# Optimization experiments

Measured on AMD Instinct MI355X. Metric: run time of the kernel, lower is better.

## Reference

```python
import jax, jax.numpy as jnp
import numpy as np

N_NODES = 50000
N_EDGES = 800000
F_IN, F_HID, F_OUT = 128, 256, 10


def setup_inputs() -> dict:
    key = jax.random.key(0)
    ks = jax.random.split(key, 8)
    x = jax.random.normal(ks[0], (N_NODES, F_IN), dtype=jnp.float32)
    edge_index = jax.random.randint(ks[1], (2, N_EDGES), 0, N_NODES, dtype=jnp.int64)
    # Glorot-ish init for GCNConv weights (PyG GCNConv: lin weight [in,out] + bias [out])
    def glorot(k, fi, fo):
        s = (6.0 / (fi + fo)) ** 0.5
        return jax.random.uniform(k, (fi, fo), minval=-s, maxval=s, dtype=jnp.float32)
    return {
        "x": x,
        "edge_index": edge_index,
        "W1": glorot(ks[2], F_IN, F_HID), "b1": jnp.zeros((F_HID,), jnp.float32),
        "W2": glorot(ks[3], F_HID, F_HID), "b2": jnp.zeros((F_HID,), jnp.float32),
        "W3": glorot(ks[4], F_HID, F_OUT), "b3": jnp.zeros((F_OUT,), jnp.float32),
    }


def _gcn_conv(x, W, b, src, dst, norm, n_nodes):
    # GCNConv: out[dst] += norm_e * (x @ W)[src]; then + bias
    xw = x @ W                                   # [N, F_out]
    msgs = norm[:, None] * xw[src]               # [E+N, F_out] gather
    agg = jax.ops.segment_sum(msgs, dst, num_segments=n_nodes)
    return agg + b


def reference(x, edge_index, W1, b1, W2, b2, W3, b3):
    n = x.shape[0]
    loops = jnp.arange(n, dtype=edge_index.dtype)
    src = jnp.concatenate([edge_index[0], loops])  # source nodes (messages from)
    dst = jnp.concatenate([edge_index[1], loops])  # target nodes (aggregate into)
    # symmetric normalization D^{-1/2} (A+I) D^{-1/2}, degree from target index
    deg = jax.ops.segment_sum(jnp.ones_like(dst, dtype=x.dtype), dst, num_segments=n)
    dinv = jnp.where(deg > 0, jax.lax.rsqrt(deg), 0.0)
    norm = dinv[src] * dinv[dst]

    h = _gcn_conv(x, W1, b1, src, dst, norm, n)
    h = jax.nn.relu(h)                  # dropout is identity in eval mode
    h = _gcn_conv(h, W2, b2, src, dst, norm, n)
    h = jax.nn.relu(h)
    h = _gcn_conv(h, W3, b3, src, dst, norm, n)
    return jax.nn.log_softmax(h, axis=1)
```

## Files before the change

### kernel.cpp

```cpp
#include <hip/hip_runtime.h>
#include <hip/hip_bf16.h>
#include <math.h>

#define F_IN 128
#define F_HID 256
#define F_OUT 10

typedef __attribute__((ext_vector_type(4))) short s16x4;
typedef __attribute__((ext_vector_type(8))) short s16x8;
typedef __attribute__((ext_vector_type(4))) float f32x4;

static __device__ __forceinline__ float b2f(unsigned short u) {
    union { float f; unsigned int u; } c;
    c.u = ((unsigned int)u) << 16;
    return c.f;
}
static __device__ __forceinline__ unsigned short f2b(float f) {
    return __bfloat16_as_ushort(__float2bfloat16(f));
}


__global__ void count_kernel(const int* __restrict__ dst, int* __restrict__ cnt, int e) {
    int i = blockIdx.x * blockDim.x + threadIdx.x;
    if (i < e) atomicAdd(&cnt[dst[i]], 1);
}

__global__ void dinv_kernel(const int* __restrict__ cnt, float* __restrict__ dinv, int n) {
    int i = blockIdx.x * blockDim.x + threadIdx.x;
    if (i < n) dinv[i] = rsqrtf((float)(cnt[i] + 1));
}

__global__ void scan1_kernel(const int* __restrict__ cnt, int* __restrict__ rowstart,
                             int* __restrict__ partial, int n) {
    __shared__ int s[256];
    int tid = threadIdx.x;
    int i = blockIdx.x * 256 + tid;
    int v = (i < n) ? cnt[i] : 0;
    s[tid] = v;
    __syncthreads();
    for (int off = 1; off < 256; off <<= 1) {
        int t = (tid >= off) ? s[tid - off] : 0;
        __syncthreads();
        s[tid] += t;
        __syncthreads();
    }
    if (i < n) rowstart[i] = s[tid] - v;
    if (tid == 255) partial[blockIdx.x] = s[255];
}

__global__ void scan2_kernel(int* __restrict__ partial, int nb) {
    __shared__ int s[256];
    int tid = threadIdx.x;
    int v = (tid < nb) ? partial[tid] : 0;
    s[tid] = v;
    __syncthreads();
    for (int off = 1; off < 256; off <<= 1) {
        int t = (tid >= off) ? s[tid - off] : 0;
        __syncthreads();
        s[tid] += t;
        __syncthreads();
    }
    if (tid < nb) partial[tid] = s[tid] - v;
}

__global__ void scan3_kernel(int* __restrict__ rowstart, const int* __restrict__ partial,
                             int n, int e) {
    int i = blockIdx.x * blockDim.x + threadIdx.x;
    if (i < n) rowstart[i] += partial[blockIdx.x];
    if (i == 0) rowstart[n] = e;
}

__global__ void fill_kernel(const int* __restrict__ src, const int* __restrict__ dst,
                            const int* __restrict__ rowstart, int* __restrict__ cursor,
                            const float* __restrict__ dinv, int* __restrict__ csr_src,
                            float* __restrict__ csr_norm, int e) {
    int i = blockIdx.x * blockDim.x + threadIdx.x;
    if (i >= e) return;
    int s = src[i], d = dst[i];
    int pos = rowstart[d] + atomicAdd(&cursor[d], 1);
    csr_src[pos] = s;
    csr_norm[pos] = dinv[s] * dinv[d];
}


__global__ void cast_kernel(const float* __restrict__ in, unsigned short* __restrict__ out,
                            size_t total) {
    size_t i = (size_t)(blockIdx.x * blockDim.x + threadIdx.x) * 4;
    if (i >= total) return;
    float4 v = *(const float4*)&in[i];
    ushort4 o;
    o.x = f2b(v.x); o.y = f2b(v.y); o.z = f2b(v.z); o.w = f2b(v.w);
    *(ushort4*)&out[i] = o;
}

__global__ void castT_kernel(const float* __restrict__ in, unsigned short* __restrict__ out,
                             int Kd, int Nd) {
    int i = blockIdx.x * blockDim.x + threadIdx.x;
    if (i >= Kd * Nd) return;
    int k = i / Nd, nn = i - k * Nd;
    out[nn * Kd + k] = f2b(in[i]);
}


template <int F>
__global__ __launch_bounds__(256) void agg_bf16_kernel(const unsigned short* __restrict__ feat,
                                                       const int* __restrict__ rowstart,
                                                       const int* __restrict__ csr_src,
                                                       const float* __restrict__ csr_norm,
                                                       const float* __restrict__ dinv,
                                                       unsigned short* __restrict__ out, int n) {
    constexpr int VEC = F / 64;
    int wid = threadIdx.x >> 6;
    int lane = threadIdx.x & 63;
    int v = blockIdx.x * 4 + wid;
    if (v >= n) return;

    float d = dinv[v];
    float sw = d * d;
    float acc[VEC];

    auto loadrow = [&](int node, float (&dst)[VEC]) {
        const unsigned short* p = feat + (size_t)node * F + lane * VEC;
        if constexpr (VEC == 4) {
            ushort4 t = *(const ushort4*)p;
            dst[0] = b2f(t.x); dst[1] = b2f(t.y); dst[2] = b2f(t.z); dst[3] = b2f(t.w);
        } else {
            ushort2 t = *(const ushort2*)p;
            dst[0] = b2f(t.x); dst[1] = b2f(t.y);
        }
    };

    {
        float t[VEC];
        loadrow(v, t);
#pragma unroll
        for (int j = 0; j < VEC; ++j) acc[j] = sw * t[j];
    }

    int e0 = rowstart[v], e1 = rowstart[v + 1];
    int e = e0;
    for (; e + 8 <= e1; e += 8) {
        int s[8];
        float w[8];
#pragma unroll
        for (int u = 0; u < 8; ++u) {
            s[u] = csr_src[e + u];
            w[u] = csr_norm[e + u];
        }
        float fv[8][VEC];
#pragma unroll
        for (int u = 0; u < 8; ++u) loadrow(s[u], fv[u]);
#pragma unroll
        for (int u = 0; u < 8; ++u)
#pragma unroll
            for (int j = 0; j < VEC; ++j) acc[j] += w[u] * fv[u][j];
    }
    for (; e + 4 <= e1; e += 4) {
        int s[4];
        float w[4];
#pragma unroll
        for (int u = 0; u < 4; ++u) {
            s[u] = csr_src[e + u];
            w[u] = csr_norm[e + u];
        }
        float fv[4][VEC];
#pragma unroll
        for (int u = 0; u < 4; ++u) loadrow(s[u], fv[u]);
#pragma unroll
        for (int u = 0; u < 4; ++u)
#pragma unroll
            for (int j = 0; j < VEC; ++j) acc[j] += w[u] * fv[u][j];
    }
    for (; e < e1; ++e) {
        int s = csr_src[e];
        float w = csr_norm[e];
        float fv[VEC];
        loadrow(s, fv);
#pragma unroll
        for (int j = 0; j < VEC; ++j) acc[j] += w * fv[j];
    }

    unsigned short* po = out + (size_t)v * F + lane * VEC;
    if constexpr (VEC == 4) {
        ushort4 o;
        o.x = f2b(acc[0]); o.y = f2b(acc[1]); o.z = f2b(acc[2]); o.w = f2b(acc[3]);
        *(ushort4*)po = o;
    } else {
        ushort2 o;
        o.x = f2b(acc[0]); o.y = f2b(acc[1]);
        *(ushort2*)po = o;
    }
}


template <int K, bool RELU, bool BF16OUT>
__global__ __launch_bounds__(256) void gemm_mfma_kernel(const unsigned short* __restrict__ A,
                                                        const unsigned short* __restrict__ Bt,
                                                        const float* __restrict__ bias,
                                                        float* __restrict__ C,
                                                        unsigned short* __restrict__ Cb,
                                                        int M, int N) {
    __shared__ unsigned short As[64][40];
    __shared__ unsigned short Bs[64][40];
    int tid = threadIdx.x;
    int w = tid >> 6;
    int lane = tid & 63;
    int g = lane >> 4;
    int r16 = lane & 15;
    int bm = blockIdx.x, bn = blockIdx.y;

    int srow = tid >> 2;
    int scol = (tid & 3) * 8;
    int garow = bm * 64 + srow;
    int gbrow = bn * 64 + srow;

    f32x4 acc[4] = {};

    for (int k0 = 0; k0 < K; k0 += 32) {
        uint4 av = make_uint4(0, 0, 0, 0);
        if (garow < M) av = *(const uint4*)&A[(size_t)garow * K + k0 + scol];
        uint4 bv = *(const uint4*)&Bt[(size_t)gbrow * K + k0 + scol];
        __syncthreads();
        *(uint4*)&As[srow][scol] = av;
        *(uint4*)&Bs[srow][scol] = bv;
        __syncthreads();

        union U { s16x8 v; s16x4 h[2]; };
        U af;
        int arow = w * 16 + r16;
        af.h[0] = *(const s16x4*)&As[arow][g * 4];
        af.h[1] = *(const s16x4*)&As[arow][g * 4 + 16];
#pragma unroll
        for (int cg = 0; cg < 4; ++cg) {
            U bf;
            bf.h[0] = *(const s16x4*)&Bs[cg * 16 + r16][g * 4];
            bf.h[1] = *(const s16x4*)&Bs[cg * 16 + r16][g * 4 + 16];
            acc[cg] = __builtin_amdgcn_mfma_f32_16x16x32_bf16(af.v, bf.v, acc[cg], 0, 0, 0);
        }
    }

#pragma unroll
    for (int cg = 0; cg < 4; ++cg) {
        int col = bn * 64 + cg * 16 + r16;
        float bs = bias[col];
#pragma unroll
        for (int r = 0; r < 4; ++r) {
            int row = bm * 64 + w * 16 + g * 4 + r;
            if (row < M) {
                float v = acc[cg][r] + bs;
                if (RELU) v = fmaxf(v, 0.f);
                if (BF16OUT) {
                    Cb[(size_t)row * N + col] = f2b(v);
                } else {
                    C[(size_t)row * N + col] = v;
                }
            }
        }
    }
}


__global__ void gemm3_kernel(const float* __restrict__ h, const float* __restrict__ W3,
                             float* __restrict__ hw3, int M) {
    __shared__ float w[F_HID * F_OUT];
    for (int i = threadIdx.x; i < F_HID * F_OUT; i += blockDim.x) w[i] = W3[i];
    __syncthreads();
    int r = blockIdx.x * blockDim.x + threadIdx.x;
    if (r >= M) return;
    float acc[F_OUT] = {};
    const float* row = &h[(size_t)r * F_HID];
    for (int k = 0; k < F_HID; k += 4) {
        float4 hv = *(const float4*)&row[k];
#pragma unroll
        for (int j = 0; j < F_OUT; ++j) {
            acc[j] += hv.x * w[(k + 0) * F_OUT + j];
            acc[j] += hv.y * w[(k + 1) * F_OUT + j];
            acc[j] += hv.z * w[(k + 2) * F_OUT + j];
            acc[j] += hv.w * w[(k + 3) * F_OUT + j];
        }
    }
#pragma unroll
    for (int j = 0; j < F_OUT; ++j) hw3[(size_t)r * F_OUT + j] = acc[j];
}


__global__ void final_kernel(const float* __restrict__ hw3, const int* __restrict__ rowstart,
                             const int* __restrict__ csr_src, const float* __restrict__ csr_norm,
                             const float* __restrict__ dinv, const float* __restrict__ b3,
                             float* __restrict__ out, int n) {
    int v = blockIdx.x * blockDim.x + threadIdx.x;
    if (v >= n) return;
    float acc[F_OUT];
    float d = dinv[v];
    float sw = d * d;
#pragma unroll
    for (int j = 0; j < F_OUT; ++j) acc[j] = sw * hw3[(size_t)v * F_OUT + j];
    int e0 = rowstart[v], e1 = rowstart[v + 1];
    for (int e = e0; e < e1; ++e) {
        int s = csr_src[e];
        float w = csr_norm[e];
#pragma unroll
        for (int j = 0; j < F_OUT; ++j) acc[j] += w * hw3[(size_t)s * F_OUT + j];
    }
#pragma unroll
    for (int j = 0; j < F_OUT; ++j) acc[j] += b3[j];
    float m = acc[0];
#pragma unroll
    for (int j = 1; j < F_OUT; ++j) m = fmaxf(m, acc[j]);
    float sum = 0.f;
#pragma unroll
    for (int j = 0; j < F_OUT; ++j) sum += expf(acc[j] - m);
    float lse = m + logf(sum);
#pragma unroll
    for (int j = 0; j < F_OUT; ++j) out[(size_t)v * F_OUT + j] = acc[j] - lse;
}


extern "C" void kernel_launch(void* const* d_in, const int* in_sizes, int n_in,
                              void* d_out, int out_size, void* d_ws, size_t ws_size,
                              hipStream_t stream) {
    const float* x  = (const float*)d_in[0];
    const int*   ei = (const int*)d_in[1];
    const float* W1 = (const float*)d_in[2];
    const float* b1 = (const float*)d_in[3];
    const float* W2 = (const float*)d_in[4];
    const float* b2 = (const float*)d_in[5];
    const float* W3 = (const float*)d_in[6];
    const float* b3 = (const float*)d_in[7];
    float* out = (float*)d_out;

    int n = in_sizes[0] / F_IN;
    int e = in_sizes[1] / 2;
    const int* srcp = ei;
    const int* dstp = ei + e;

    size_t off = 0;
    auto alloc = [&](size_t bytes) -> char* {
        char* p = (char*)d_ws + off;
        off += (bytes + 255) & ~(size_t)255;
        return p;
    };
    int*   cnt      = (int*)alloc((size_t)n * 4);
    int*   cursor   = (int*)alloc((size_t)n * 4);
    int*   rowstart = (int*)alloc((size_t)(n + 1) * 4);
    int*   partial  = (int*)alloc(1024 * 4);
    int*   csr_src  = (int*)alloc((size_t)e * 4);
    float* csr_norm = (float*)alloc((size_t)e * 4);
    float* dinv     = (float*)alloc((size_t)n * 4);
    unsigned short* xb   = (unsigned short*)alloc((size_t)n * F_IN * 2);
    unsigned short* aggb = (unsigned short*)alloc((size_t)n * F_HID * 2);
    unsigned short* h1b  = (unsigned short*)alloc((size_t)n * F_HID * 2);
    unsigned short* W1t  = (unsigned short*)alloc((size_t)F_IN * F_HID * 2);
    unsigned short* W2t  = (unsigned short*)alloc((size_t)F_HID * F_HID * 2);
    float* h2  = (float*)alloc((size_t)n * F_HID * 4);
    float* hw3 = (float*)alloc((size_t)n * F_OUT * 4);

    const int TB = 256;
    hipMemsetAsync(cnt, 0, (size_t)n * 4, stream);
    hipMemsetAsync(cursor, 0, (size_t)n * 4, stream);

    count_kernel<<<(e + TB - 1) / TB, TB, 0, stream>>>(dstp, cnt, e);
    dinv_kernel<<<(n + TB - 1) / TB, TB, 0, stream>>>(cnt, dinv, n);
    int nb = (n + TB - 1) / TB;
    scan1_kernel<<<nb, TB, 0, stream>>>(cnt, rowstart, partial, n);
    scan2_kernel<<<1, TB, 0, stream>>>(partial, nb);
    scan3_kernel<<<nb, TB, 0, stream>>>(rowstart, partial, n, e);
    fill_kernel<<<(e + TB - 1) / TB, TB, 0, stream>>>(srcp, dstp, rowstart, cursor, dinv,
                                                      csr_src, csr_norm, e);

    size_t xtotal = (size_t)n * F_IN;
    cast_kernel<<<(int)((xtotal / 4 + TB - 1) / TB), TB, 0, stream>>>(x, xb, xtotal);
    castT_kernel<<<(F_IN * F_HID + TB - 1) / TB, TB, 0, stream>>>(W1, W1t, F_IN, F_HID);
    castT_kernel<<<(F_HID * F_HID + TB - 1) / TB, TB, 0, stream>>>(W2, W2t, F_HID, F_HID);

    int nwave = (n + 3) / 4;
    dim3 gg((n + 63) / 64, F_HID / 64);

    agg_bf16_kernel<F_IN><<<nwave, 256, 0, stream>>>(xb, rowstart, csr_src, csr_norm, dinv,
                                                     aggb, n);
    gemm_mfma_kernel<F_IN, true, true><<<gg, 256, 0, stream>>>(aggb, W1t, b1, nullptr, h1b,
                                                               n, F_HID);

    agg_bf16_kernel<F_HID><<<nwave, 256, 0, stream>>>(h1b, rowstart, csr_src, csr_norm, dinv,
                                                      aggb, n);
    gemm_mfma_kernel<F_HID, true, false><<<gg, 256, 0, stream>>>(aggb, W2t, b2, h2, nullptr,
                                                                 n, F_HID);

    gemm3_kernel<<<(n + TB - 1) / TB, TB, 0, stream>>>(h2, W3, hw3, n);
    final_kernel<<<(n + TB - 1) / TB, TB, 0, stream>>>(hw3, rowstart, csr_src, csr_norm, dinv,
                                                       b3, out, n);
}
```

Before: 282.6 us.

## Fuse prep kernels, pack CSR src/norm, and split aggregation across feature chunks

Merges the degree count, the x cast and both weight transposes into one multi-job launch, and folds the dinv computation into the first scan pass. The memsets are merged into one, relying on cursor directly following cnt in the workspace. CSR source indices and norms are interleaved into one int2 array. Aggregation now launches a grid over 32-feature column slices, with four edge lanes per feature pair that are reduced by shuffles. This is meant to cut launch count and raise parallelism in the gather, at the cost of re-reading the edge list once per feature slice.

```diff
diff --git a/kernel.cpp b/kernel.cpp
--- a/kernel.cpp
+++ b/kernel.cpp
@@ -20,18 +20,38 @@
 }
 
 
-__global__ void count_kernel(const int* __restrict__ dst, int* __restrict__ cnt, int e) {
+__global__ void prep_kernel(const int* __restrict__ dst, int* __restrict__ cnt, int e,
+                            const float* __restrict__ x, unsigned short* __restrict__ xb,
+                            int xq,
+                            const float* __restrict__ W1, unsigned short* __restrict__ W1t,
+                            const float* __restrict__ W2, unsigned short* __restrict__ W2t) {
     int i = blockIdx.x * blockDim.x + threadIdx.x;
-    if (i < e) atomicAdd(&cnt[dst[i]], 1);
-}
-
-__global__ void dinv_kernel(const int* __restrict__ cnt, float* __restrict__ dinv, int n) {
-    int i = blockIdx.x * blockDim.x + threadIdx.x;
-    if (i < n) dinv[i] = rsqrtf((float)(cnt[i] + 1));
-}
+    int job = blockIdx.y;
+    if (job == 0) {
+        if (i < e) atomicAdd(&cnt[dst[i]], 1);
+    } else if (job == 1) {
+        if (i < xq) {
+            float4 v = *(const float4*)&x[(size_t)i * 4];
+            ushort4 o;
+            o.x = f2b(v.x); o.y = f2b(v.y); o.z = f2b(v.z); o.w = f2b(v.w);
+            *(ushort4*)&xb[(size_t)i * 4] = o;
+        }
+    } else if (job == 2) {
+        if (i < F_IN * F_HID) {
+            int k = i / F_HID, nn = i - k * F_HID;
+            W1t[nn * F_IN + k] = f2b(W1[i]);
+        }
+    } else {
+        if (i < F_HID * F_HID) {
+            int k = i / F_HID, nn = i - k * F_HID;
+            W2t[nn * F_HID + k] = f2b(W2[i]);
+        }
+    }
+}
+
 
 __global__ void scan1_kernel(const int* __restrict__ cnt, int* __restrict__ rowstart,
-                             int* __restrict__ partial, int n) {
+                             int* __restrict__ partial, float* __restrict__ dinv, int n) {
     __shared__ int s[256];
     int tid = threadIdx.x;
     int i = blockIdx.x * 256 + tid;
@@ -44,7 +64,10 @@
         s[tid] += t;
         __syncthreads();
     }
-    if (i < n) rowstart[i] = s[tid] - v;
+    if (i < n) {
+        rowstart[i] = s[tid] - v;
+        dinv[i] = rsqrtf((float)(v + 1));
+    }
     if (tid == 255) partial[blockIdx.x] = s[255];
 }
 
@@ -72,123 +95,69 @@
 
 __global__ void fill_kernel(const int* __restrict__ src, const int* __restrict__ dst,
                             const int* __restrict__ rowstart, int* __restrict__ cursor,
-                            const float* __restrict__ dinv, int* __restrict__ csr_src,
-                            float* __restrict__ csr_norm, int e) {
+                            const float* __restrict__ dinv, int2* __restrict__ pack, int e) {
     int i = blockIdx.x * blockDim.x + threadIdx.x;
     if (i >= e) return;
     int s = src[i], d = dst[i];
     int pos = rowstart[d] + atomicAdd(&cursor[d], 1);
-    csr_src[pos] = s;
-    csr_norm[pos] = dinv[s] * dinv[d];
-}
-
-
-__global__ void cast_kernel(const float* __restrict__ in, unsigned short* __restrict__ out,
-                            size_t total) {
-    size_t i = (size_t)(blockIdx.x * blockDim.x + threadIdx.x) * 4;
-    if (i >= total) return;
-    float4 v = *(const float4*)&in[i];
-    ushort4 o;
-    o.x = f2b(v.x); o.y = f2b(v.y); o.z = f2b(v.z); o.w = f2b(v.w);
-    *(ushort4*)&out[i] = o;
-}
-
-__global__ void castT_kernel(const float* __restrict__ in, unsigned short* __restrict__ out,
-                             int Kd, int Nd) {
-    int i = blockIdx.x * blockDim.x + threadIdx.x;
-    if (i >= Kd * Nd) return;
-    int k = i / Nd, nn = i - k * Nd;
-    out[nn * Kd + k] = f2b(in[i]);
+    float w = dinv[s] * dinv[d];
+    pack[pos] = make_int2(s, __float_as_int(w));
 }
 
 
 template <int F>
-__global__ __launch_bounds__(256) void agg_bf16_kernel(const unsigned short* __restrict__ feat,
-                                                       const int* __restrict__ rowstart,
-                                                       const int* __restrict__ csr_src,
-                                                       const float* __restrict__ csr_norm,
-                                                       const float* __restrict__ dinv,
-                                                       unsigned short* __restrict__ out, int n) {
-    constexpr int VEC = F / 64;
+__global__ __launch_bounds__(256) void agg_split_kernel(const unsigned short* __restrict__ feat,
+                                                        const int* __restrict__ rowstart,
+                                                        const int2* __restrict__ pack,
+                                                        const float* __restrict__ dinv,
+                                                        unsigned short* __restrict__ out,
+                                                        int n) {
     int wid = threadIdx.x >> 6;
     int lane = threadIdx.x & 63;
     int v = blockIdx.x * 4 + wid;
     if (v >= n) return;
+    int esub = lane >> 4;
+    int fidx = lane & 15;
+    int fbase = blockIdx.y * 32;
+    const unsigned short* fcol = feat + fbase + fidx * 2;
 
     float d = dinv[v];
-    float sw = d * d;
-    float acc[VEC];
-
-    auto loadrow = [&](int node, float (&dst)[VEC]) {
-        const unsigned short* p = feat + (size_t)node * F + lane * VEC;
-        if constexpr (VEC == 4) {
-            ushort4 t = *(const ushort4*)p;
-            dst[0] = b2f(t.x); dst[1] = b2f(t.y); dst[2] = b2f(t.z); dst[3] = b2f(t.w);
-        } else {
-            ushort2 t = *(const ushort2*)p;
-            dst[0] = b2f(t.x); dst[1] = b2f(t.y);
-        }
-    };
-
+    float sw = (esub == 0) ? d * d : 0.f;
+    float a0, a1;
     {
-        float t[VEC];
-        loadrow(v, t);
-#pragma unroll
-        for (int j = 0; j < VEC; ++j) acc[j] = sw * t[j];
+        ushort2 t = *(const ushort2*)&fcol[(size_t)v * F];
+        a0 = sw * b2f(t.x);
+        a1 = sw * b2f(t.y);
     }
 
     int e0 = rowstart[v], e1 = rowstart[v + 1];
-    int e = e0;
-    for (; e + 8 <= e1; e += 8) {
-        int s[8];
-        float w[8];
-#pragma unroll
-        for (int u = 0; u < 8; ++u) {
-            s[u] = csr_src[e + u];
-            w[u] = csr_norm[e + u];
-        }
-        float fv[8][VEC];
-#pragma unroll
-        for (int u = 0; u < 8; ++u) loadrow(s[u], fv[u]);
-#pragma unroll
-        for (int u = 0; u < 8; ++u)
-#pragma unroll
-            for (int j = 0; j < VEC; ++j) acc[j] += w[u] * fv[u][j];
-    }
-    for (; e + 4 <= e1; e += 4) {
-        int s[4];
-        float w[4];
-#pragma unroll
-        for (int u = 0; u < 4; ++u) {
-            s[u] = csr_src[e + u];
-            w[u] = csr_norm[e + u];
-        }
-        float fv[4][VEC];
-#pragma unroll
-        for (int u = 0; u < 4; ++u) loadrow(s[u], fv[u]);
-#pragma unroll
-        for (int u = 0; u < 4; ++u)
-#pragma unroll
-            for (int j = 0; j < VEC; ++j) acc[j] += w[u] * fv[u][j];
-    }
-    for (; e < e1; ++e) {
-        int s = csr_src[e];
-        float w = csr_norm[e];
-        float fv[VEC];
-        loadrow(s, fv);
-#pragma unroll
-        for (int j = 0; j < VEC; ++j) acc[j] += w * fv[j];
-    }
-
-    unsigned short* po = out + (size_t)v * F + lane * VEC;
-    if constexpr (VEC == 4) {
-        ushort4 o;
-        o.x = f2b(acc[0]); o.y = f2b(acc[1]); o.z = f2b(acc[2]); o.w = f2b(acc[3]);
-        *(ushort4*)po = o;
-    } else {
+    for (int e = e0; e < e1; e += 8) {
+        int ea = e + esub;
+        int eb = e + 4 + esub;
+        bool oka = ea < e1;
+        bool okb = eb < e1;
+        int2 pa = pack[oka ? ea : e];
+        int2 pb = pack[okb ? eb : e];
+        float wa = oka ? __int_as_float(pa.y) : 0.f;
+        float wb = okb ? __int_as_float(pb.y) : 0.f;
+        ushort2 ta = *(const ushort2*)&fcol[(size_t)pa.x * F];
+        ushort2 tb = *(const ushort2*)&fcol[(size_t)pb.x * F];
+        a0 += wa * b2f(ta.x);
+        a1 += wa * b2f(ta.y);
+        a0 += wb * b2f(tb.x);
+        a1 += wb * b2f(tb.y);
+    }
+
+    a0 += __shfl_xor(a0, 16);
+    a1 += __shfl_xor(a1, 16);
+    a0 += __shfl_xor(a0, 32);
+    a1 += __shfl_xor(a1, 32);
+
+    if (esub == 0) {
         ushort2 o;
-        o.x = f2b(acc[0]); o.y = f2b(acc[1]);
-        *(ushort2*)po = o;
+        o.x = f2b(a0);
+        o.y = f2b(a1);
+        *(ushort2*)&out[(size_t)v * F + fbase + fidx * 2] = o;
     }
 }
 
@@ -285,9 +254,8 @@
 
 
 __global__ void final_kernel(const float* __restrict__ hw3, const int* __restrict__ rowstart,
-                             const int* __restrict__ csr_src, const float* __restrict__ csr_norm,
-                             const float* __restrict__ dinv, const float* __restrict__ b3,
-                             float* __restrict__ out, int n) {
+                             const int2* __restrict__ pack, const float* __restrict__ dinv,
+                             const float* __restrict__ b3, float* __restrict__ out, int n) {
     int v = blockIdx.x * blockDim.x + threadIdx.x;
     if (v >= n) return;
     float acc[F_OUT];
@@ -297,10 +265,10 @@
     for (int j = 0; j < F_OUT; ++j) acc[j] = sw * hw3[(size_t)v * F_OUT + j];
     int e0 = rowstart[v], e1 = rowstart[v + 1];
     for (int e = e0; e < e1; ++e) {
-        int s = csr_src[e];
-        float w = csr_norm[e];
-#pragma unroll
-        for (int j = 0; j < F_OUT; ++j) acc[j] += w * hw3[(size_t)s * F_OUT + j];
+        int2 p = pack[e];
+        float w = __int_as_float(p.y);
+#pragma unroll
+        for (int j = 0; j < F_OUT; ++j) acc[j] += w * hw3[(size_t)p.x * F_OUT + j];
     }
 #pragma unroll
     for (int j = 0; j < F_OUT; ++j) acc[j] += b3[j];
@@ -340,12 +308,12 @@
         off += (bytes + 255) & ~(size_t)255;
         return p;
     };
+    size_t cntpad = ((size_t)n * 4 + 255) & ~(size_t)255;
     int*   cnt      = (int*)alloc((size_t)n * 4);
     int*   cursor   = (int*)alloc((size_t)n * 4);
     int*   rowstart = (int*)alloc((size_t)(n + 1) * 4);
     int*   partial  = (int*)alloc(1024 * 4);
-    int*   csr_src  = (int*)alloc((size_t)e * 4);
-    float* csr_norm = (float*)alloc((size_t)e * 4);
+    int2*  pack     = (int2*)alloc((size_t)e * 8);
     float* dinv     = (float*)alloc((size_t)n * 4);
     unsigned short* xb   = (unsigned short*)alloc((size_t)n * F_IN * 2);
     unsigned short* aggb = (unsigned short*)alloc((size_t)n * F_HID * 2);
@@ -356,37 +324,33 @@
     float* hw3 = (float*)alloc((size_t)n * F_OUT * 4);
 
     const int TB = 256;
-    hipMemsetAsync(cnt, 0, (size_t)n * 4, stream);
-    hipMemsetAsync(cursor, 0, (size_t)n * 4, stream);
-
-    count_kernel<<<(e + TB - 1) / TB, TB, 0, stream>>>(dstp, cnt, e);
-    dinv_kernel<<<(n + TB - 1) / TB, TB, 0, stream>>>(cnt, dinv, n);
+    hipMemsetAsync(cnt, 0, cntpad + (size_t)n * 4, stream);
+
+    int xq = (int)((size_t)n * F_IN / 4);
+    int prepmax = e > xq ? e : xq;
+    dim3 gp((prepmax + TB - 1) / TB, 4);
+    prep_kernel<<<gp, TB, 0, stream>>>(dstp, cnt, e, x, xb, xq, W1, W1t, W2, W2t);
+
     int nb = (n + TB - 1) / TB;
-    scan1_kernel<<<nb, TB, 0, stream>>>(cnt, rowstart, partial, n);
+    scan1_kernel<<<nb, TB, 0, stream>>>(cnt, rowstart, partial, dinv, n);
     scan2_kernel<<<1, TB, 0, stream>>>(partial, nb);
     scan3_kernel<<<nb, TB, 0, stream>>>(rowstart, partial, n, e);
     fill_kernel<<<(e + TB - 1) / TB, TB, 0, stream>>>(srcp, dstp, rowstart, cursor, dinv,
-                                                      csr_src, csr_norm, e);
-
-    size_t xtotal = (size_t)n * F_IN;
-    cast_kernel<<<(int)((xtotal / 4 + TB - 1) / TB), TB, 0, stream>>>(x, xb, xtotal);
-    castT_kernel<<<(F_IN * F_HID + TB - 1) / TB, TB, 0, stream>>>(W1, W1t, F_IN, F_HID);
-    castT_kernel<<<(F_HID * F_HID + TB - 1) / TB, TB, 0, stream>>>(W2, W2t, F_HID, F_HID);
+                                                      pack, e);
 
     int nwave = (n + 3) / 4;
     dim3 gg((n + 63) / 64, F_HID / 64);
-
-    agg_bf16_kernel<F_IN><<<nwave, 256, 0, stream>>>(xb, rowstart, csr_src, csr_norm, dinv,
-                                                     aggb, n);
+    dim3 ga1(nwave, F_IN / 32);
+    dim3 ga2(nwave, F_HID / 32);
+
+    agg_split_kernel<F_IN><<<ga1, 256, 0, stream>>>(xb, rowstart, pack, dinv, aggb, n);
     gemm_mfma_kernel<F_IN, true, true><<<gg, 256, 0, stream>>>(aggb, W1t, b1, nullptr, h1b,
                                                                n, F_HID);
 
-    agg_bf16_kernel<F_HID><<<nwave, 256, 0, stream>>>(h1b, rowstart, csr_src, csr_norm, dinv,
-                                                      aggb, n);
+    agg_split_kernel<F_HID><<<ga2, 256, 0, stream>>>(h1b, rowstart, pack, dinv, aggb, n);
     gemm_mfma_kernel<F_HID, true, false><<<gg, 256, 0, stream>>>(aggb, W2t, b2, h2, nullptr,
                                                                  n, F_HID);
 
     gemm3_kernel<<<(n + TB - 1) / TB, TB, 0, stream>>>(h2, W3, hw3, n);
-    final_kernel<<<(n + TB - 1) / TB, TB, 0, stream>>>(hw3, rowstart, csr_src, csr_norm, dinv,
-                                                       b3, out, n);
-}
+    final_kernel<<<(n + TB - 1) / TB, TB, 0, stream>>>(hw3, rowstart, pack, dinv, b3, out, n);
+}
```

Result: slower. 398.4 us (+41.0%).
